# Kernel tuning notes

Hardware: AMD Instinct MI355X
Metric: run time of the kernel (lower is better)

The kernel has to match this reference:

```python
import jax, jax.numpy as jnp
import numpy as np

B, S, H = 2, 2048, 1024
E, K, I, IS = 8, 2, 1408, 2816

def setup_inputs() -> dict:
    key = jax.random.key(0)
    ks = jax.random.split(key, 9)
    sc = lambda fan_in: 1.0 / np.sqrt(fan_in)
    return {
        'hidden_states': jax.random.normal(ks[0], (B, S, H), jnp.float32),
        'gate_w': jax.random.normal(ks[1], (H, E), jnp.float32) * sc(H),
        'w_gate': jax.random.normal(ks[2], (E, H, I), jnp.float32) * sc(H),
        'w_up': jax.random.normal(ks[3], (E, H, I), jnp.float32) * sc(H),
        'w_down': jax.random.normal(ks[4], (E, I, H), jnp.float32) * sc(I),
        'sh_gate_w': jax.random.normal(ks[5], (H, IS), jnp.float32) * sc(H),
        'sh_up_w': jax.random.normal(ks[6], (H, IS), jnp.float32) * sc(H),
        'sh_down_w': jax.random.normal(ks[7], (IS, H), jnp.float32) * sc(IS),
        'sh_expert_gate_w': jax.random.normal(ks[8], (H, 1), jnp.float32) * sc(H),
        'top_k': K,
    }

def reference(hidden_states, gate_w, w_gate, w_up, w_down, sh_gate_w, sh_up_w, sh_down_w, sh_expert_gate_w, top_k):
    orig_shape = hidden_states.shape
    x = hidden_states.reshape(-1, orig_shape[-1])  # [T, H]
    T = x.shape[0]
    n_experts = gate_w.shape[1]
    # --- routing (matches _route_single_token, no expert_bias) ---
    logits = x @ gate_w                               # [T, E]
    topk_vals, topk_ids = jax.lax.top_k(logits, top_k)  # [T, K]
    topk_weights = jax.nn.softmax(topk_vals, axis=-1)   # [T, K]
    # dense routing matrix [T, E]; each token has K nonzeros
    route = jnp.zeros((T, n_experts), x.dtype).at[jnp.arange(T)[:, None], topk_ids].add(topk_weights)
    # --- expert SwiGLU FFNs, masked-combine over the fixed expert set ---
    out = jnp.zeros_like(x)
    for e in range(n_experts):
        h = jax.nn.silu(x @ w_gate[e]) * (x @ w_up[e])  # [T, I]
        out = out + route[:, e:e + 1] * (h @ w_down[e])
    # --- shared expert (always active) with sigmoid gate ---
    shared = (jax.nn.silu(x @ sh_gate_w) * (x @ sh_up_w)) @ sh_down_w
    shared = jax.nn.sigmoid(x @ sh_expert_gate_w) * shared
    out = out + shared
    return out.reshape(orig_shape)
```

## Files before the change

### kernel.cpp

```cpp
#include <hip/hip_runtime.h>
#include <hip/hip_bf16.h>

#define T_TOK 4096
#define HDIM  1024
#define NEXP  8
#define IDIM  1408
#define ISDIM 2816

typedef short bf16x8 __attribute__((ext_vector_type(8)));
typedef float f32x4  __attribute__((ext_vector_type(4)));
typedef unsigned short u16;
typedef unsigned short u16x4 __attribute__((ext_vector_type(4)));
typedef unsigned short u16x8 __attribute__((ext_vector_type(8)));

typedef __attribute__((address_space(1))) const void gvoid;
typedef __attribute__((address_space(3))) void lvoid;

__device__ __forceinline__ u16 f2bf(float f) {
    union { float f; unsigned u; } c; c.f = f;
    unsigned r = (c.u + 0x7FFFu + ((c.u >> 16) & 1u)) >> 16;
    return (u16)r;
}
__device__ __forceinline__ float bf2f(u16 v) {
    union { unsigned u; float f; } c; c.u = (unsigned)v << 16; return c.f;
}
__device__ __forceinline__ void glds16(const u16* g, u16* l) {
    __builtin_amdgcn_global_load_lds((gvoid*)g, (lvoid*)l, 16, 0, 0);
}

__global__ __launch_bounds__(256) void route_kernel(
    const float* __restrict__ X, const float* __restrict__ GW,
    const float* __restrict__ SEG,
    int* __restrict__ topk_e, float* __restrict__ topk_w,
    float* __restrict__ sgate)
{
    const int t = blockIdx.x * 4 + (threadIdx.x >> 6);
    const int lane = threadIdx.x & 63;
    float acc[NEXP];
    #pragma unroll
    for (int e = 0; e < NEXP; ++e) acc[e] = 0.f;
    float sacc = 0.f;
    const float* xr = X + (size_t)t * HDIM;
    for (int h = lane; h < HDIM; h += 64) {
        float xv = xr[h];
        f32x4 g0 = *(const f32x4*)(GW + (size_t)h * NEXP);
        f32x4 g1 = *(const f32x4*)(GW + (size_t)h * NEXP + 4);
        acc[0] += xv * g0[0]; acc[1] += xv * g0[1];
        acc[2] += xv * g0[2]; acc[3] += xv * g0[3];
        acc[4] += xv * g1[0]; acc[5] += xv * g1[1];
        acc[6] += xv * g1[2]; acc[7] += xv * g1[3];
        sacc += xv * SEG[h];
    }
    #pragma unroll
    for (int off = 32; off > 0; off >>= 1) {
        #pragma unroll
        for (int e = 0; e < NEXP; ++e) acc[e] += __shfl_down(acc[e], off);
        sacc += __shfl_down(sacc, off);
    }
    if (lane == 0) {
        int e0 = 0;
        #pragma unroll
        for (int e = 1; e < NEXP; ++e) if (acc[e] > acc[e0]) e0 = e;
        int e1 = (e0 == 0) ? 1 : 0;
        #pragma unroll
        for (int e = 0; e < NEXP; ++e)
            if (e != e0 && acc[e] > acc[e1]) e1 = e;
        float w0 = 1.f / (1.f + __expf(acc[e1] - acc[e0]));
        topk_e[t * 2]     = e0; topk_e[t * 2 + 1] = e1;
        topk_w[t * 2]     = w0; topk_w[t * 2 + 1] = 1.f - w0;
        sgate[t] = 1.f / (1.f + __expf(-sacc));
    }
}

__global__ __launch_bounds__(256) void hist_kernel(
    const int* __restrict__ topk_e, int* __restrict__ counts)
{
    __shared__ int h[NEXP];
    if (threadIdx.x < NEXP) h[threadIdx.x] = 0;
    __syncthreads();
    int i = blockIdx.x * 256 + threadIdx.x;
    atomicAdd(&h[topk_e[i]], 1);
    __syncthreads();
    if (threadIdx.x < NEXP) atomicAdd(&counts[threadIdx.x], h[threadIdx.x]);
}

__global__ void offsets_kernel(const int* __restrict__ counts,
                               int* __restrict__ seg_start,
                               int* __restrict__ cursors)
{
    if (threadIdx.x == 0) {
        int s = 0;
        for (int e = 0; e < NEXP; ++e) {
            seg_start[e] = s; cursors[e] = s; s += counts[e];
        }
    }
}

__global__ __launch_bounds__(256) void scatter_kernel(
    const int* __restrict__ topk_e,
    int* __restrict__ cursors, int* __restrict__ tok_ids,
    int* __restrict__ slot)
{
    const int i = blockIdx.x * 256 + threadIdx.x;
    const int lane = threadIdx.x & 63;
    const int e = topk_e[i];
    const unsigned long long lt = (1ull << lane) - 1ull;
    #pragma unroll
    for (int ex = 0; ex < NEXP; ++ex) {
        unsigned long long mask = __ballot(e == ex);
        if (mask == 0ull) continue;
        int cnt = __popcll(mask);
        int leader = __ffsll((long long)mask) - 1;
        int base_ = 0;
        if (lane == leader) base_ = atomicAdd(&cursors[ex], cnt);
        base_ = __shfl(base_, leader);
        if (e == ex) {
            int pos = base_ + __popcll(mask & lt);
            tok_ids[pos] = i >> 1;
            slot[i] = pos;
        }
    }
}

__global__ __launch_bounds__(256) void cvt_x_kernel(
    const float* __restrict__ in, u16* __restrict__ out, int n)
{
    int i = (blockIdx.x * 256 + threadIdx.x) * 8;
    if (i < n) {
        f32x4 a = *(const f32x4*)(in + i);
        f32x4 b = *(const f32x4*)(in + i + 4);
        u16x8 o;
        #pragma unroll
        for (int j = 0; j < 4; ++j) { o[j] = f2bf(a[j]); o[j + 4] = f2bf(b[j]); }
        *(u16x8*)(out + i) = o;
    }
}

__global__ __launch_bounds__(256) void transpose_cvt(
    const float* __restrict__ in0, const float* __restrict__ in1,
    u16* __restrict__ out, int K, int N, int split)
{
    const int z = blockIdx.z;
    const float* in = (z < split) ? (in0 + (size_t)z * K * N)
                                  : (in1 + (size_t)(z - split) * K * N);
    u16* o = out + (size_t)z * N * K;

    __shared__ float tile[64][65];
    const int n0 = blockIdx.x * 64, k0 = blockIdx.y * 64;
    const int tx = threadIdx.x & 15;
    const int ty = threadIdx.x >> 4;

    #pragma unroll
    for (int p = 0; p < 4; ++p) {
        int k = ty + p * 16;
        f32x4 v = *(const f32x4*)(in + (size_t)(k0 + k) * N + n0 + tx * 4);
        *(f32x4*)&tile[k][tx * 4] = v;
    }
    __syncthreads();
    #pragma unroll
    for (int p = 0; p < 4; ++p) {
        int n = ty + p * 16;
        u16x4 w;
        #pragma unroll
        for (int j = 0; j < 4; ++j) w[j] = f2bf(tile[tx * 4 + j][n]);
        *(u16x4*)(o + (size_t)(n0 + n) * K + k0 + tx * 4) = w;
    }
}

__global__ __launch_bounds__(256) void gemm_gu(
    const u16* __restrict__ A,
    const u16* __restrict__ Bg_, const u16* __restrict__ Bu_, size_t b_stride,
    u16* __restrict__ Hout,
    const int* __restrict__ a_ids, const int* __restrict__ seg_start,
    const int* __restrict__ counts,
    int N, int Trows)
{
    int e, m_tile, cnt, base;
    if (counts) {
        e = blockIdx.x; m_tile = blockIdx.y;
        cnt = counts[e]; base = seg_start[e];
    } else {
        e = 0; m_tile = blockIdx.x * gridDim.y + blockIdx.y;
        cnt = Trows; base = 0;
    }
    const int m0 = m_tile * 128;
    if (m0 >= cnt) return;
    const int n0 = blockIdx.z * 64;
    const u16* Bg = Bg_ + (size_t)e * b_stride;
    const u16* Bu = Bu_ + (size_t)e * b_stride;
    const int K = HDIM;

    __shared__ u16 As[2 * 4096];
    __shared__ u16 Bs[2 * 4096];

    const int tid = threadIdx.x;
    const int srow = tid >> 2;
    const int st_k = (tid & 3) * 8;
    int ar0 = m0 + srow;       if (ar0 >= cnt) ar0 = cnt - 1;
    int ar1 = m0 + srow + 64;  if (ar1 >= cnt) ar1 = cnt - 1;
    const int ga0 = a_ids ? a_ids[base + ar0] : (base + ar0);
    const int ga1 = a_ids ? a_ids[base + ar1] : (base + ar1);
    const u16* a0 = A + (size_t)ga0 * K + st_k;
    const u16* a1 = A + (size_t)ga1 * K + st_k;
    const u16* bg = Bg + (size_t)(n0 + srow) * K + st_k;
    const u16* bu = Bu + (size_t)(n0 + srow) * K + st_k;

    f32x4 accG[4][2], accU[4][2];
    #pragma unroll
    for (int i = 0; i < 4; ++i)
        #pragma unroll
        for (int j = 0; j < 2; ++j) {
            accG[i][j] = (f32x4){0.f, 0.f, 0.f, 0.f};
            accU[i][j] = (f32x4){0.f, 0.f, 0.f, 0.f};
        }

    const int lane = tid & 63;
    const int wv = tid >> 6;
    const int wr = (wv >> 1) * 64;
    const int wc = (wv & 1) * 32;
    const int lrow = lane & 15;
    const int lkb = (lane >> 4) * 8;

    int offA[4], offBg[2];
    #pragma unroll
    for (int m = 0; m < 4; ++m) offA[m] = (wr + m * 16 + lrow) * 32 + lkb;
    #pragma unroll
    for (int n = 0; n < 2; ++n) offBg[n] = (wc + n * 16 + lrow) * 32 + lkb;

#define STAGE_GU(ps) do { \
    glds16(a0, &As[(ps) + tid * 8]); \
    glds16(a1, &As[(ps) + 2048 + tid * 8]); \
    glds16(bg, &Bs[(ps) + tid * 8]); \
    glds16(bu, &Bs[(ps) + 2048 + tid * 8]); \
    a0 += 32; a1 += 32; bg += 32; bu += 32; } while (0)

#define COMPUTE_GU(ps) do { \
    bf16x8 af[4], bgf[2], bux[2]; \
    _Pragma("unroll") for (int m = 0; m < 4; ++m) af[m] = *(const bf16x8*)&As[(ps) + offA[m]]; \
    _Pragma("unroll") for (int n = 0; n < 2; ++n) { \
        bgf[n] = *(const bf16x8*)&Bs[(ps) + offBg[n]]; \
        bux[n] = *(const bf16x8*)&Bs[(ps) + offBg[n] + 2048]; } \
    _Pragma("unroll") for (int m = 0; m < 4; ++m) \
        _Pragma("unroll") for (int n = 0; n < 2; ++n) { \
            accG[m][n] = __builtin_amdgcn_mfma_f32_16x16x32_bf16(af[m], bgf[n], accG[m][n], 0, 0, 0); \
            accU[m][n] = __builtin_amdgcn_mfma_f32_16x16x32_bf16(af[m], bux[n], accU[m][n], 0, 0, 0); } \
    } while (0)

    STAGE_GU(0);
    STAGE_GU(4096);
    #pragma unroll 1
    for (int t = 0; t < 30; ++t) {
        asm volatile("s_waitcnt vmcnt(4)" ::: "memory");
        __builtin_amdgcn_s_barrier();
        const int ps = (t & 1) * 4096;
        COMPUTE_GU(ps);
        __builtin_amdgcn_s_barrier();
        STAGE_GU(ps);
    }
    asm volatile("s_waitcnt vmcnt(4)" ::: "memory");
    __builtin_amdgcn_s_barrier();
    COMPUTE_GU(0);
    asm volatile("s_waitcnt vmcnt(0)" ::: "memory");
    __builtin_amdgcn_s_barrier();
    COMPUTE_GU(4096);

    const int l4 = (lane >> 4) * 4;
    #pragma unroll
    for (int m = 0; m < 4; ++m)
        #pragma unroll
        for (int n = 0; n < 2; ++n)
            #pragma unroll
            for (int j = 0; j < 4; ++j) {
                int r = wr + m * 16 + l4 + j;
                if (m0 + r < cnt) {
                    int c = n0 + wc + n * 16 + lrow;
                    float g = accG[m][n][j], u = accU[m][n][j];
                    float hv = g / (1.f + __expf(-g)) * u;
                    Hout[(size_t)(base + m0 + r) * N + c] = f2bf(hv);
                }
            }
}

__global__ __launch_bounds__(256) void gemm_down(
    const u16* __restrict__ AE, const u16* __restrict__ AS,
    const u16* __restrict__ WDt, const u16* __restrict__ SDt,
    float* __restrict__ DexpO, float* __restrict__ OutS,
    const int* __restrict__ seg_start, const int* __restrict__ counts)
{
    const int zz = blockIdx.x;
    const bool shr = (zz >= 64);
    int n0, cnt, base, kstride;
    size_t koff;
    const u16 *Ab, *Be;
    if (!shr) {
        int e = zz & 7;
        n0 = (zz >> 3) * 128;
        cnt = counts[e]; base = seg_start[e];
        Ab = AE; Be = WDt + (size_t)e * (HDIM * IDIM);
        kstride = IDIM; koff = 0;
    } else {
        int idx = zz - 64;
        n0 = (idx & 7) * 128;
        cnt = T_TOK; base = 0;
        Ab = AS; Be = SDt;
        kstride = ISDIM; koff = (size_t)(idx >> 3) * 1408;
    }
    const int m0 = blockIdx.y * 128;
    if (m0 >= cnt) return;
    const int NT = 44;

    __shared__ u16 As[2 * 4096];
    __shared__ u16 Bs[2 * 4096];

    const int tid = threadIdx.x;
    const int srow = tid >> 2;
    const int st_k = (tid & 3) * 8;
    int ar0 = m0 + srow;       if (ar0 >= cnt) ar0 = cnt - 1;
    int ar1 = m0 + srow + 64;  if (ar1 >= cnt) ar1 = cnt - 1;
    const u16* a0 = Ab + (size_t)(base + ar0) * kstride + koff + st_k;
    const u16* a1 = Ab + (size_t)(base + ar1) * kstride + koff + st_k;
    const u16* b0 = Be + (size_t)(n0 + srow) * kstride + koff + st_k;
    const u16* b1 = Be + (size_t)(n0 + srow + 64) * kstride + koff + st_k;

    f32x4 acc[4][4];
    #pragma unroll
    for (int i = 0; i < 4; ++i)
        #pragma unroll
        for (int j = 0; j < 4; ++j) acc[i][j] = (f32x4){0.f, 0.f, 0.f, 0.f};

    const int lane = tid & 63;
    const int wv = tid >> 6;
    const int wr = (wv >> 1) * 64;
    const int wc = (wv & 1) * 64;
    const int lrow = lane & 15;
    const int lkb = (lane >> 4) * 8;

    int offA[4], offB[4];
    #pragma unroll
    for (int m = 0; m < 4; ++m) offA[m] = (wr + m * 16 + lrow) * 32 + lkb;
    #pragma unroll
    for (int n = 0; n < 4; ++n) offB[n] = (wc + n * 16 + lrow) * 32 + lkb;

#define STAGE_DN(ps) do { \
    glds16(a0, &As[(ps) + tid * 8]); \
    glds16(a1, &As[(ps) + 2048 + tid * 8]); \
    glds16(b0, &Bs[(ps) + tid * 8]); \
    glds16(b1, &Bs[(ps) + 2048 + tid * 8]); \
    a0 += 32; a1 += 32; b0 += 32; b1 += 32; } while (0)

#define COMPUTE_DN(ps) do { \
    bf16x8 af[4], bff[4]; \
    _Pragma("unroll") for (int m = 0; m < 4; ++m) af[m] = *(const bf16x8*)&As[(ps) + offA[m]]; \
    _Pragma("unroll") for (int n = 0; n < 4; ++n) bff[n] = *(const bf16x8*)&Bs[(ps) + offB[n]]; \
    _Pragma("unroll") for (int m = 0; m < 4; ++m) \
        _Pragma("unroll") for (int n = 0; n < 4; ++n) \
            acc[m][n] = __builtin_amdgcn_mfma_f32_16x16x32_bf16(af[m], bff[n], acc[m][n], 0, 0, 0); \
    } while (0)

    STAGE_DN(0);
    STAGE_DN(4096);
    #pragma unroll 1
    for (int t = 0; t < NT - 2; ++t) {
        asm volatile("s_waitcnt vmcnt(4)" ::: "memory");
        __builtin_amdgcn_s_barrier();
        const int ps = (t & 1) * 4096;
        COMPUTE_DN(ps);
        __builtin_amdgcn_s_barrier();
        STAGE_DN(ps);
    }
    asm volatile("s_waitcnt vmcnt(4)" ::: "memory");
    __builtin_amdgcn_s_barrier();
    COMPUTE_DN(0);
    asm volatile("s_waitcnt vmcnt(0)" ::: "memory");
    __builtin_amdgcn_s_barrier();
    COMPUTE_DN(4096);

    const int l4 = (lane >> 4) * 4;
    #pragma unroll
    for (int m = 0; m < 4; ++m)
        #pragma unroll
        for (int n = 0; n < 4; ++n)
            #pragma unroll
            for (int j = 0; j < 4; ++j) {
                int r = wr + m * 16 + l4 + j;
                if (m0 + r < cnt) {
                    int c = n0 + wc + n * 16 + lrow;
                    if (!shr)
                        DexpO[(size_t)(base + m0 + r) * HDIM + c] = acc[m][n][j];
                    else
                        atomicAdd(&OutS[(size_t)(m0 + r) * HDIM + c], acc[m][n][j]);
                }
            }
}

__global__ __launch_bounds__(256) void combine_kernel(
    const float* __restrict__ Dexp,
    const int* __restrict__ slot, const float* __restrict__ topk_w,
    const float* __restrict__ sgate, float* __restrict__ Out)
{
    int idx = blockIdx.x * 256 + threadIdx.x;
    int t = idx >> 8;
    int c = (idx & 255) * 4;
    int s0 = slot[2 * t], s1 = slot[2 * t + 1];
    float w0 = topk_w[2 * t], w1 = topk_w[2 * t + 1], sg = sgate[t];
    f32x4 sh = *(const f32x4*)(Out + (size_t)t * HDIM + c);
    f32x4 d0 = *(const f32x4*)(Dexp + (size_t)s0 * HDIM + c);
    f32x4 d1 = *(const f32x4*)(Dexp + (size_t)s1 * HDIM + c);
    f32x4 o;
    #pragma unroll
    for (int j = 0; j < 4; ++j) o[j] = sg * sh[j] + w0 * d0[j] + w1 * d1[j];
    *(f32x4*)(Out + (size_t)t * HDIM + c) = o;
}

extern "C" void kernel_launch(void* const* d_in, const int* in_sizes, int n_in,
                              void* d_out, int out_size, void* d_ws, size_t ws_size,
                              hipStream_t stream)
{
    const float* X   = (const float*)d_in[0];
    const float* GW  = (const float*)d_in[1];
    const float* WG  = (const float*)d_in[2];
    const float* WU  = (const float*)d_in[3];
    const float* WD  = (const float*)d_in[4];
    const float* SG  = (const float*)d_in[5];
    const float* SU  = (const float*)d_in[6];
    const float* SD  = (const float*)d_in[7];
    const float* SEG = (const float*)d_in[8];
    float* Out = (float*)d_out;

    char* ws = (char*)d_ws;
    int*   counts    = (int*)(ws + 0);
    int*   seg_start = (int*)(ws + 64);
    int*   cursors   = (int*)(ws + 128);
    int*   topk_e    = (int*)(ws + 1024);
    float* topk_w    = (float*)(ws + 1024 + 32768);
    float* sgate     = (float*)(ws + 1024 + 65536);
    int*   tok_ids   = (int*)(ws + 1024 + 65536 + 16384);
    int*   slot      = (int*)(ws + 1024 + 65536 + 16384 + 32768);

    u16* Xbf  = (u16*)(ws + 0x40000ull);
    u16* Hact = (u16*)(ws + 0xA00000ull);
    u16* Hs   = (u16*)(ws + 0x2200000ull);
    u16* WGUt = (u16*)(ws + 0x3A00000ull);
    u16* WDt  = (u16*)(ws + 0x6900000ull);
    u16* SGUt = (u16*)(ws + 0x8100000ull);
    u16* SDt  = (u16*)(ws + 0x8D00000ull);
    u16* WGt = WGUt;
    u16* WUt = WGUt + (size_t)NEXP * IDIM * HDIM;
    u16* SGt = SGUt;
    u16* SUt = SGUt + (size_t)ISDIM * HDIM;
    float* Dexp = (float*)(ws + 0x3A00000ull);

    hipMemsetAsync(counts, 0, 64, stream);
    hipMemsetAsync(Out, 0, (size_t)T_TOK * HDIM * sizeof(float), stream);

    route_kernel<<<T_TOK / 4, 256, 0, stream>>>(X, GW, SEG, topk_e, topk_w, sgate);
    hist_kernel<<<(T_TOK * 2) / 256, 256, 0, stream>>>(topk_e, counts);
    offsets_kernel<<<1, 64, 0, stream>>>(counts, seg_start, cursors);
    scatter_kernel<<<(T_TOK * 2) / 256, 256, 0, stream>>>(topk_e, cursors, tok_ids, slot);

    cvt_x_kernel<<<(T_TOK * HDIM) / (256 * 8), 256, 0, stream>>>(X, Xbf, T_TOK * HDIM);
    transpose_cvt<<<dim3(IDIM / 64, HDIM / 64, 2 * NEXP), 256, 0, stream>>>(WG, WU, WGUt, HDIM, IDIM, NEXP);
    transpose_cvt<<<dim3(HDIM / 64, IDIM / 64, NEXP), 256, 0, stream>>>(WD, WD, WDt, IDIM, HDIM, NEXP);
    transpose_cvt<<<dim3(ISDIM / 64, HDIM / 64, 2), 256, 0, stream>>>(SG, SU, SGUt, HDIM, ISDIM, 1);
    transpose_cvt<<<dim3(HDIM / 64, ISDIM / 64, 1), 256, 0, stream>>>(SD, SD, SDt, ISDIM, HDIM, 1);

    gemm_gu<<<dim3(NEXP, T_TOK / 128, IDIM / 64), 256, 0, stream>>>(
        Xbf, WGt, WUt, (size_t)IDIM * HDIM, Hact,
        tok_ids, seg_start, counts, IDIM, 0);
    gemm_gu<<<dim3(8, T_TOK / 128 / 8, ISDIM / 64), 256, 0, stream>>>(
        Xbf, SGt, SUt, 0, Hs,
        nullptr, nullptr, nullptr, ISDIM, T_TOK);

    gemm_down<<<dim3(80, T_TOK / 128), 256, 0, stream>>>(
        Hact, Hs, WDt, SDt, Dexp, Out,
        seg_start, counts);

    combine_kernel<<<(T_TOK * HDIM / 4) / 256, 256, 0, stream>>>(
        Dexp, slot, topk_w, sgate, Out);
}
```

Before: 342.4 us.

## Enlarge GEMM tiles to 256x256 with interleaved gate/up weights and swizzled LDS

The gate/up and down GEMMs move from 128-row tiles with 256 threads to 256x256 tiles with 512 threads, BK=64 and a 128KB dynamic LDS double buffer. Gate and up weight rows are interleaved in 16-row groups during the transpose, so a single B tile carries both, and the epilogue pairs adjacent fragments for SwiGLU. LDS reads use an XOR swizzle to avoid bank conflicts, and MFMA bursts run at raised wave priority. The aim is more reuse per loaded byte and fewer tiles, at the cost of more padding waste on small expert segments, higher register pressure and lower occupancy.

```diff
diff --git a/kernel.cpp b/kernel.cpp
--- a/kernel.cpp
+++ b/kernel.cpp
@@ -138,12 +138,15 @@
 
 __global__ __launch_bounds__(256) void transpose_cvt(
     const float* __restrict__ in0, const float* __restrict__ in1,
-    u16* __restrict__ out, int K, int N, int split)
+    u16* __restrict__ out, int K, int N, int split, int ilv)
 {
     const int z = blockIdx.z;
+    const int e = (z < split) ? z : z - split;
     const float* in = (z < split) ? (in0 + (size_t)z * K * N)
                                   : (in1 + (size_t)(z - split) * K * N);
-    u16* o = out + (size_t)z * N * K;
+    u16* o = ilv ? (out + (size_t)e * 2 * N * K)
+                 : (out + (size_t)z * N * K);
+    const int radd = ilv ? ((z < split) ? 0 : 16) : 0;
 
     __shared__ float tile[64][65];
     const int n0 = blockIdx.x * 64, k0 = blockIdx.y * 64;
@@ -163,232 +166,228 @@
         u16x4 w;
         #pragma unroll
         for (int j = 0; j < 4; ++j) w[j] = f2bf(tile[tx * 4 + j][n]);
-        *(u16x4*)(o + (size_t)(n0 + n) * K + k0 + tx * 4) = w;
-    }
-}
-
-__global__ __launch_bounds__(256) void gemm_gu(
-    const u16* __restrict__ A,
-    const u16* __restrict__ Bg_, const u16* __restrict__ Bu_, size_t b_stride,
+        int R = n0 + n;
+        int orow = ilv ? (((R >> 4) * 32) + (R & 15) + radd) : R;
+        *(u16x4*)(o + (size_t)orow * K + k0 + tx * 4) = w;
+    }
+}
+
+
+#define MFMA16(MB, AV, BV) \
+    _Pragma("unroll") for (int m_ = 0; m_ < 4; ++m_) \
+        _Pragma("unroll") for (int n_ = 0; n_ < 4; ++n_) \
+            acc[(MB) + m_][n_] = __builtin_amdgcn_mfma_f32_16x16x32_bf16(AV[m_], BV[n_], acc[(MB) + m_][n_], 0, 0, 0);
+
+#define COMP256(bufo) do { \
+    bf16x8 av[4], bv[4]; \
+    _Pragma("unroll") for (int m_ = 0; m_ < 4; ++m_) av[m_] = *(const bf16x8*)&As[(bufo) + aof + m_ * 1024]; \
+    _Pragma("unroll") for (int n_ = 0; n_ < 4; ++n_) bv[n_] = *(const bf16x8*)&Bs[(bufo) + bof + n_ * 1024]; \
+    __builtin_amdgcn_s_setprio(1); MFMA16(0, av, bv) __builtin_amdgcn_s_setprio(0); \
+    _Pragma("unroll") for (int m_ = 0; m_ < 4; ++m_) av[m_] = *(const bf16x8*)&As[(bufo) + aof + (m_ + 4) * 1024]; \
+    __builtin_amdgcn_s_setprio(1); MFMA16(4, av, bv) __builtin_amdgcn_s_setprio(0); \
+    _Pragma("unroll") for (int m_ = 0; m_ < 4; ++m_) av[m_] = *(const bf16x8*)&As[(bufo) + (aof ^ 32) + m_ * 1024]; \
+    _Pragma("unroll") for (int n_ = 0; n_ < 4; ++n_) bv[n_] = *(const bf16x8*)&Bs[(bufo) + (bof ^ 32) + n_ * 1024]; \
+    __builtin_amdgcn_s_setprio(1); MFMA16(0, av, bv) __builtin_amdgcn_s_setprio(0); \
+    _Pragma("unroll") for (int m_ = 0; m_ < 4; ++m_) av[m_] = *(const bf16x8*)&As[(bufo) + (aof ^ 32) + (m_ + 4) * 1024]; \
+    __builtin_amdgcn_s_setprio(1); MFMA16(4, av, bv) __builtin_amdgcn_s_setprio(0); \
+} while (0)
+
+#define STAGE256() do { \
+    glds16(ap0, &As[stbuf + tid * 8]); \
+    glds16(ap1, &As[stbuf + 4096 + tid * 8]); \
+    glds16(ap2, &As[stbuf + 8192 + tid * 8]); \
+    glds16(ap3, &As[stbuf + 12288 + tid * 8]); \
+    glds16(bp0, &Bs[stbuf + tid * 8]); \
+    glds16(bp1, &Bs[stbuf + 4096 + tid * 8]); \
+    glds16(bp2, &Bs[stbuf + 8192 + tid * 8]); \
+    glds16(bp3, &Bs[stbuf + 12288 + tid * 8]); \
+    ap0 += 64; ap1 += 64; ap2 += 64; ap3 += 64; \
+    bp0 += 64; bp1 += 64; bp2 += 64; bp3 += 64; \
+    stbuf ^= 16384; } while (0)
+
+#define GEMM_LOOP(NT) \
+    STAGE256(); STAGE256(); \
+    _Pragma("unroll 1") \
+    for (int t = 0; t < (NT) - 2; ++t) { \
+        asm volatile("s_waitcnt vmcnt(8)" ::: "memory"); \
+        __builtin_amdgcn_s_barrier(); \
+        COMP256((t & 1) * 16384); \
+        __builtin_amdgcn_s_barrier(); \
+        STAGE256(); \
+    } \
+    asm volatile("s_waitcnt vmcnt(8)" ::: "memory"); \
+    __builtin_amdgcn_s_barrier(); \
+    COMP256(0); \
+    asm volatile("s_waitcnt vmcnt(0)" ::: "memory"); \
+    __builtin_amdgcn_s_barrier(); \
+    COMP256(16384);
+
+__global__ __launch_bounds__(512, 2) void gemm_gu(
+    const u16* __restrict__ A, const u16* __restrict__ Bc_, size_t b_stride,
     u16* __restrict__ Hout,
     const int* __restrict__ a_ids, const int* __restrict__ seg_start,
-    const int* __restrict__ counts,
-    int N, int Trows)
-{
-    int e, m_tile, cnt, base;
+    const int* __restrict__ counts, int Nout)
+{
+    extern __shared__ u16 lds[];
+    u16* As = lds;
+    u16* Bs = lds + 32768;
+
+    int e, m0, cnt, base;
     if (counts) {
-        e = blockIdx.x; m_tile = blockIdx.y;
+        e = blockIdx.x; m0 = blockIdx.y * 256;
         cnt = counts[e]; base = seg_start[e];
     } else {
-        e = 0; m_tile = blockIdx.x * gridDim.y + blockIdx.y;
-        cnt = Trows; base = 0;
-    }
-    const int m0 = m_tile * 128;
+        e = 0; m0 = (blockIdx.x * gridDim.y + blockIdx.y) * 256;
+        cnt = T_TOK; base = 0;
+    }
     if (m0 >= cnt) return;
-    const int n0 = blockIdx.z * 64;
-    const u16* Bg = Bg_ + (size_t)e * b_stride;
-    const u16* Bu = Bu_ + (size_t)e * b_stride;
+    const u16* Bsrc = Bc_ + (size_t)e * b_stride;
     const int K = HDIM;
-
-    __shared__ u16 As[2 * 4096];
-    __shared__ u16 Bs[2 * 4096];
+    const int n0e = blockIdx.z * 256;
 
     const int tid = threadIdx.x;
-    const int srow = tid >> 2;
-    const int st_k = (tid & 3) * 8;
-    int ar0 = m0 + srow;       if (ar0 >= cnt) ar0 = cnt - 1;
-    int ar1 = m0 + srow + 64;  if (ar1 >= cnt) ar1 = cnt - 1;
-    const int ga0 = a_ids ? a_ids[base + ar0] : (base + ar0);
-    const int ga1 = a_ids ? a_ids[base + ar1] : (base + ar1);
-    const u16* a0 = A + (size_t)ga0 * K + st_k;
-    const u16* a1 = A + (size_t)ga1 * K + st_k;
-    const u16* bg = Bg + (size_t)(n0 + srow) * K + st_k;
-    const u16* bu = Bu + (size_t)(n0 + srow) * K + st_k;
-
-    f32x4 accG[4][2], accU[4][2];
-    #pragma unroll
-    for (int i = 0; i < 4; ++i)
-        #pragma unroll
-        for (int j = 0; j < 2; ++j) {
-            accG[i][j] = (f32x4){0.f, 0.f, 0.f, 0.f};
-            accU[i][j] = (f32x4){0.f, 0.f, 0.f, 0.f};
-        }
+    const int srow = tid >> 3;
+    const int sw = ((tid & 7) ^ (srow & 7)) * 8;
+
+    const u16 *ap0, *ap1, *ap2, *ap3, *bp0, *bp1, *bp2, *bp3;
+    {
+        int r0 = m0 + srow;       if (r0 >= cnt) r0 = cnt - 1;
+        int r1 = m0 + 64 + srow;  if (r1 >= cnt) r1 = cnt - 1;
+        int r2 = m0 + 128 + srow; if (r2 >= cnt) r2 = cnt - 1;
+        int r3 = m0 + 192 + srow; if (r3 >= cnt) r3 = cnt - 1;
+        int g0 = a_ids ? a_ids[base + r0] : (base + r0);
+        int g1 = a_ids ? a_ids[base + r1] : (base + r1);
+        int g2 = a_ids ? a_ids[base + r2] : (base + r2);
+        int g3 = a_ids ? a_ids[base + r3] : (base + r3);
+        ap0 = A + (size_t)g0 * K + sw;
+        ap1 = A + (size_t)g1 * K + sw;
+        ap2 = A + (size_t)g2 * K + sw;
+        ap3 = A + (size_t)g3 * K + sw;
+        bp0 = Bsrc + (size_t)(n0e + srow) * K + sw;
+        bp1 = Bsrc + (size_t)(n0e + 64 + srow) * K + sw;
+        bp2 = Bsrc + (size_t)(n0e + 128 + srow) * K + sw;
+        bp3 = Bsrc + (size_t)(n0e + 192 + srow) * K + sw;
+    }
+    int stbuf = 0;
+
+    f32x4 acc[8][4];
+    #pragma unroll
+    for (int i = 0; i < 8; ++i)
+        #pragma unroll
+        for (int j = 0; j < 4; ++j) acc[i][j] = (f32x4){0.f, 0.f, 0.f, 0.f};
 
     const int lane = tid & 63;
     const int wv = tid >> 6;
-    const int wr = (wv >> 1) * 64;
-    const int wc = (wv & 1) * 32;
+    const int wr = wv >> 2;
+    const int wn = wv & 3;
     const int lrow = lane & 15;
-    const int lkb = (lane >> 4) * 8;
-
-    int offA[4], offBg[2];
-    #pragma unroll
-    for (int m = 0; m < 4; ++m) offA[m] = (wr + m * 16 + lrow) * 32 + lkb;
-    #pragma unroll
-    for (int n = 0; n < 2; ++n) offBg[n] = (wc + n * 16 + lrow) * 32 + lkb;
-
-#define STAGE_GU(ps) do { \
-    glds16(a0, &As[(ps) + tid * 8]); \
-    glds16(a1, &As[(ps) + 2048 + tid * 8]); \
-    glds16(bg, &Bs[(ps) + tid * 8]); \
-    glds16(bu, &Bs[(ps) + 2048 + tid * 8]); \
-    a0 += 32; a1 += 32; bg += 32; bu += 32; } while (0)
-
-#define COMPUTE_GU(ps) do { \
-    bf16x8 af[4], bgf[2], bux[2]; \
-    _Pragma("unroll") for (int m = 0; m < 4; ++m) af[m] = *(const bf16x8*)&As[(ps) + offA[m]]; \
-    _Pragma("unroll") for (int n = 0; n < 2; ++n) { \
-        bgf[n] = *(const bf16x8*)&Bs[(ps) + offBg[n]]; \
-        bux[n] = *(const bf16x8*)&Bs[(ps) + offBg[n] + 2048]; } \
-    _Pragma("unroll") for (int m = 0; m < 4; ++m) \
-        _Pragma("unroll") for (int n = 0; n < 2; ++n) { \
-            accG[m][n] = __builtin_amdgcn_mfma_f32_16x16x32_bf16(af[m], bgf[n], accG[m][n], 0, 0, 0); \
-            accU[m][n] = __builtin_amdgcn_mfma_f32_16x16x32_bf16(af[m], bux[n], accU[m][n], 0, 0, 0); } \
-    } while (0)
-
-    STAGE_GU(0);
-    STAGE_GU(4096);
-    #pragma unroll 1
-    for (int t = 0; t < 30; ++t) {
-        asm volatile("s_waitcnt vmcnt(4)" ::: "memory");
-        __builtin_amdgcn_s_barrier();
-        const int ps = (t & 1) * 4096;
-        COMPUTE_GU(ps);
-        __builtin_amdgcn_s_barrier();
-        STAGE_GU(ps);
-    }
-    asm volatile("s_waitcnt vmcnt(4)" ::: "memory");
-    __builtin_amdgcn_s_barrier();
-    COMPUTE_GU(0);
-    asm volatile("s_waitcnt vmcnt(0)" ::: "memory");
-    __builtin_amdgcn_s_barrier();
-    COMPUTE_GU(4096);
-
-    const int l4 = (lane >> 4) * 4;
-    #pragma unroll
-    for (int m = 0; m < 4; ++m)
-        #pragma unroll
-        for (int n = 0; n < 2; ++n)
+    const int kslot = lane >> 4;
+    const int aof = (wr * 128 + lrow) * 64 + ((kslot ^ (lrow & 7)) * 8);
+    const int bof = (wn * 64 + lrow) * 64 + ((kslot ^ (lrow & 7)) * 8);
+
+    GEMM_LOOP(16)
+
+    const int l4 = kslot * 4;
+    #pragma unroll
+    for (int mf = 0; mf < 8; ++mf)
+        #pragma unroll
+        for (int p = 0; p < 2; ++p) {
+            f32x4 g = acc[mf][2 * p], u = acc[mf][2 * p + 1];
+            int ci = blockIdx.z * 128 + (wn * 2 + p) * 16 + lrow;
             #pragma unroll
             for (int j = 0; j < 4; ++j) {
-                int r = wr + m * 16 + l4 + j;
-                if (m0 + r < cnt) {
-                    int c = n0 + wc + n * 16 + lrow;
-                    float g = accG[m][n][j], u = accU[m][n][j];
-                    float hv = g / (1.f + __expf(-g)) * u;
-                    Hout[(size_t)(base + m0 + r) * N + c] = f2bf(hv);
+                int r = m0 + wr * 128 + mf * 16 + l4 + j;
+                if (r < cnt) {
+                    float hv = g[j] / (1.f + __expf(-g[j])) * u[j];
+                    Hout[(size_t)(base + r) * Nout + ci] = f2bf(hv);
                 }
             }
-}
-
-__global__ __launch_bounds__(256) void gemm_down(
+        }
+}
+
+__global__ __launch_bounds__(512, 2) void gemm_down(
     const u16* __restrict__ AE, const u16* __restrict__ AS,
     const u16* __restrict__ WDt, const u16* __restrict__ SDt,
     float* __restrict__ DexpO, float* __restrict__ OutS,
     const int* __restrict__ seg_start, const int* __restrict__ counts)
 {
+    extern __shared__ u16 lds[];
+    u16* As = lds;
+    u16* Bs = lds + 32768;
+
     const int zz = blockIdx.x;
-    const bool shr = (zz >= 64);
-    int n0, cnt, base, kstride;
+    const bool shr = (zz >= 32);
+    int n0, cnt, base, kst;
     size_t koff;
-    const u16 *Ab, *Be;
+    const u16 *Asrc, *Bsrc;
     if (!shr) {
         int e = zz & 7;
-        n0 = (zz >> 3) * 128;
+        n0 = (zz >> 3) * 256;
         cnt = counts[e]; base = seg_start[e];
-        Ab = AE; Be = WDt + (size_t)e * (HDIM * IDIM);
-        kstride = IDIM; koff = 0;
+        Asrc = AE; Bsrc = WDt + (size_t)e * (HDIM * IDIM);
+        kst = IDIM; koff = 0;
     } else {
-        int idx = zz - 64;
-        n0 = (idx & 7) * 128;
+        int idx = zz - 32;
+        n0 = (idx & 3) * 256;
         cnt = T_TOK; base = 0;
-        Ab = AS; Be = SDt;
-        kstride = ISDIM; koff = (size_t)(idx >> 3) * 1408;
-    }
-    const int m0 = blockIdx.y * 128;
+        Asrc = AS; Bsrc = SDt;
+        kst = ISDIM; koff = (size_t)(idx >> 2) * 1408;
+    }
+    const int m0 = blockIdx.y * 256;
     if (m0 >= cnt) return;
-    const int NT = 44;
-
-    __shared__ u16 As[2 * 4096];
-    __shared__ u16 Bs[2 * 4096];
 
     const int tid = threadIdx.x;
-    const int srow = tid >> 2;
-    const int st_k = (tid & 3) * 8;
-    int ar0 = m0 + srow;       if (ar0 >= cnt) ar0 = cnt - 1;
-    int ar1 = m0 + srow + 64;  if (ar1 >= cnt) ar1 = cnt - 1;
-    const u16* a0 = Ab + (size_t)(base + ar0) * kstride + koff + st_k;
-    const u16* a1 = Ab + (size_t)(base + ar1) * kstride + koff + st_k;
-    const u16* b0 = Be + (size_t)(n0 + srow) * kstride + koff + st_k;
-    const u16* b1 = Be + (size_t)(n0 + srow + 64) * kstride + koff + st_k;
-
-    f32x4 acc[4][4];
-    #pragma unroll
-    for (int i = 0; i < 4; ++i)
+    const int srow = tid >> 3;
+    const int sw = ((tid & 7) ^ (srow & 7)) * 8;
+
+    const u16 *ap0, *ap1, *ap2, *ap3, *bp0, *bp1, *bp2, *bp3;
+    {
+        int r0 = m0 + srow;       if (r0 >= cnt) r0 = cnt - 1;
+        int r1 = m0 + 64 + srow;  if (r1 >= cnt) r1 = cnt - 1;
+        int r2 = m0 + 128 + srow; if (r2 >= cnt) r2 = cnt - 1;
+        int r3 = m0 + 192 + srow; if (r3 >= cnt) r3 = cnt - 1;
+        ap0 = Asrc + (size_t)(base + r0) * kst + koff + sw;
+        ap1 = Asrc + (size_t)(base + r1) * kst + koff + sw;
+        ap2 = Asrc + (size_t)(base + r2) * kst + koff + sw;
+        ap3 = Asrc + (size_t)(base + r3) * kst + koff + sw;
+        bp0 = Bsrc + (size_t)(n0 + srow) * kst + koff + sw;
+        bp1 = Bsrc + (size_t)(n0 + 64 + srow) * kst + koff + sw;
+        bp2 = Bsrc + (size_t)(n0 + 128 + srow) * kst + koff + sw;
+        bp3 = Bsrc + (size_t)(n0 + 192 + srow) * kst + koff + sw;
+    }
+    int stbuf = 0;
+
+    f32x4 acc[8][4];
+    #pragma unroll
+    for (int i = 0; i < 8; ++i)
         #pragma unroll
         for (int j = 0; j < 4; ++j) acc[i][j] = (f32x4){0.f, 0.f, 0.f, 0.f};
 
     const int lane = tid & 63;
     const int wv = tid >> 6;
-    const int wr = (wv >> 1) * 64;
-    const int wc = (wv & 1) * 64;
+    const int wr = wv >> 2;
+    const int wn = wv & 3;
     const int lrow = lane & 15;
-    const int lkb = (lane >> 4) * 8;
-
-    int offA[4], offB[4];
-    #pragma unroll
-    for (int m = 0; m < 4; ++m) offA[m] = (wr + m * 16 + lrow) * 32 + lkb;
-    #pragma unroll
-    for (int n = 0; n < 4; ++n) offB[n] = (wc + n * 16 + lrow) * 32 + lkb;
-
-#define STAGE_DN(ps) do { \
-    glds16(a0, &As[(ps) + tid * 8]); \
-    glds16(a1, &As[(ps) + 2048 + tid * 8]); \
-    glds16(b0, &Bs[(ps) + tid * 8]); \
-    glds16(b1, &Bs[(ps) + 2048 + tid * 8]); \
-    a0 += 32; a1 += 32; b0 += 32; b1 += 32; } while (0)
-
-#define COMPUTE_DN(ps) do { \
-    bf16x8 af[4], bff[4]; \
-    _Pragma("unroll") for (int m = 0; m < 4; ++m) af[m] = *(const bf16x8*)&As[(ps) + offA[m]]; \
-    _Pragma("unroll") for (int n = 0; n < 4; ++n) bff[n] = *(const bf16x8*)&Bs[(ps) + offB[n]]; \
-    _Pragma("unroll") for (int m = 0; m < 4; ++m) \
-        _Pragma("unroll") for (int n = 0; n < 4; ++n) \
-            acc[m][n] = __builtin_amdgcn_mfma_f32_16x16x32_bf16(af[m], bff[n], acc[m][n], 0, 0, 0); \
-    } while (0)
-
-    STAGE_DN(0);
-    STAGE_DN(4096);
-    #pragma unroll 1
-    for (int t = 0; t < NT - 2; ++t) {
-        asm volatile("s_waitcnt vmcnt(4)" ::: "memory");
-        __builtin_amdgcn_s_barrier();
-        const int ps = (t & 1) * 4096;
-        COMPUTE_DN(ps);
-        __builtin_amdgcn_s_barrier();
-        STAGE_DN(ps);
-    }
-    asm volatile("s_waitcnt vmcnt(4)" ::: "memory");
-    __builtin_amdgcn_s_barrier();
-    COMPUTE_DN(0);
-    asm volatile("s_waitcnt vmcnt(0)" ::: "memory");
-    __builtin_amdgcn_s_barrier();
-    COMPUTE_DN(4096);
-
-    const int l4 = (lane >> 4) * 4;
-    #pragma unroll
-    for (int m = 0; m < 4; ++m)
-        #pragma unroll
-        for (int n = 0; n < 4; ++n)
+    const int kslot = lane >> 4;
+    const int aof = (wr * 128 + lrow) * 64 + ((kslot ^ (lrow & 7)) * 8);
+    const int bof = (wn * 64 + lrow) * 64 + ((kslot ^ (lrow & 7)) * 8);
+
+    GEMM_LOOP(22)
+
+    const int l4 = kslot * 4;
+    #pragma unroll
+    for (int mf = 0; mf < 8; ++mf)
+        #pragma unroll
+        for (int nf = 0; nf < 4; ++nf)
             #pragma unroll
             for (int j = 0; j < 4; ++j) {
-                int r = wr + m * 16 + l4 + j;
-                if (m0 + r < cnt) {
-                    int c = n0 + wc + n * 16 + lrow;
+                int r = m0 + wr * 128 + mf * 16 + l4 + j;
+                if (r < cnt) {
+                    int c = n0 + wn * 64 + nf * 16 + lrow;
                     if (!shr)
-                        DexpO[(size_t)(base + m0 + r) * HDIM + c] = acc[m][n][j];
+                        DexpO[(size_t)(base + r) * HDIM + c] = acc[mf][nf][j];
                     else
-                        atomicAdd(&OutS[(size_t)(m0 + r) * HDIM + c], acc[m][n][j]);
+                        atomicAdd(&OutS[(size_t)r * HDIM + c], acc[mf][nf][j]);
                 }
             }
 }
@@ -440,14 +439,10 @@
     u16* Xbf  = (u16*)(ws + 0x40000ull);
     u16* Hact = (u16*)(ws + 0xA00000ull);
     u16* Hs   = (u16*)(ws + 0x2200000ull);
-    u16* WGUt = (u16*)(ws + 0x3A00000ull);
+    u16* WGUc = (u16*)(ws + 0x3A00000ull);
     u16* WDt  = (u16*)(ws + 0x6900000ull);
-    u16* SGUt = (u16*)(ws + 0x8100000ull);
+    u16* SGUc = (u16*)(ws + 0x8100000ull);
     u16* SDt  = (u16*)(ws + 0x8D00000ull);
-    u16* WGt = WGUt;
-    u16* WUt = WGUt + (size_t)NEXP * IDIM * HDIM;
-    u16* SGt = SGUt;
-    u16* SUt = SGUt + (size_t)ISDIM * HDIM;
     float* Dexp = (float*)(ws + 0x3A00000ull);
 
     hipMemsetAsync(counts, 0, 64, stream);
@@ -459,19 +454,19 @@
     scatter_kernel<<<(T_TOK * 2) / 256, 256, 0, stream>>>(topk_e, cursors, tok_ids, slot);
 
     cvt_x_kernel<<<(T_TOK * HDIM) / (256 * 8), 256, 0, stream>>>(X, Xbf, T_TOK * HDIM);
-    transpose_cvt<<<dim3(IDIM / 64, HDIM / 64, 2 * NEXP), 256, 0, stream>>>(WG, WU, WGUt, HDIM, IDIM, NEXP);
-    transpose_cvt<<<dim3(HDIM / 64, IDIM / 64, NEXP), 256, 0, stream>>>(WD, WD, WDt, IDIM, HDIM, NEXP);
-    transpose_cvt<<<dim3(ISDIM / 64, HDIM / 64, 2), 256, 0, stream>>>(SG, SU, SGUt, HDIM, ISDIM, 1);
-    transpose_cvt<<<dim3(HDIM / 64, ISDIM / 64, 1), 256, 0, stream>>>(SD, SD, SDt, ISDIM, HDIM, 1);
-
-    gemm_gu<<<dim3(NEXP, T_TOK / 128, IDIM / 64), 256, 0, stream>>>(
-        Xbf, WGt, WUt, (size_t)IDIM * HDIM, Hact,
-        tok_ids, seg_start, counts, IDIM, 0);
-    gemm_gu<<<dim3(8, T_TOK / 128 / 8, ISDIM / 64), 256, 0, stream>>>(
-        Xbf, SGt, SUt, 0, Hs,
-        nullptr, nullptr, nullptr, ISDIM, T_TOK);
-
-    gemm_down<<<dim3(80, T_TOK / 128), 256, 0, stream>>>(
+    transpose_cvt<<<dim3(IDIM / 64, HDIM / 64, 2 * NEXP), 256, 0, stream>>>(WG, WU, WGUc, HDIM, IDIM, NEXP, 1);
+    transpose_cvt<<<dim3(HDIM / 64, IDIM / 64, NEXP), 256, 0, stream>>>(WD, WD, WDt, IDIM, HDIM, NEXP, 0);
+    transpose_cvt<<<dim3(ISDIM / 64, HDIM / 64, 2), 256, 0, stream>>>(SG, SU, SGUc, HDIM, ISDIM, 1, 1);
+    transpose_cvt<<<dim3(HDIM / 64, ISDIM / 64, 1), 256, 0, stream>>>(SD, SD, SDt, ISDIM, HDIM, 1, 0);
+
+    gemm_gu<<<dim3(NEXP, 16, 11), 512, 131072, stream>>>(
+        Xbf, WGUc, (size_t)2 * IDIM * HDIM, Hact,
+        tok_ids, seg_start, counts, IDIM);
+    gemm_gu<<<dim3(8, 2, 22), 512, 131072, stream>>>(
+        Xbf, SGUc, 0, Hs,
+        nullptr, nullptr, nullptr, ISDIM);
+
+    gemm_down<<<dim3(40, 16), 512, 131072, stream>>>(
         Hact, Hs, WDt, SDt, Dexp, Out,
         seg_start, counts);
 
```

Result: slower. 363.2 us (+6.1%).

## Triple-buffer LDS staging and XOR-swizzle k-chunks in both MoE GEMMs

Applied to the files above, without the earlier changes.

Both the gate/up GEMM and the down GEMM move from double to triple LDS buffering, which keeps two k-tiles of global-to-LDS loads in flight (vmcnt 8) while the current tile is computed. The loop tail is extended so the last three tiles drain correctly. The 8-element k-chunk positions are XOR-swizzled by row on the global load side and matched on the fragment read side, so MFMA operand reads from LDS should hit fewer bank conflicts. The cost is 1.5x the shared memory per block (48KB), which may lower occupancy, plus modulo-3 buffer indexing.

```diff
diff --git a/kernel.cpp b/kernel.cpp
--- a/kernel.cpp
+++ b/kernel.cpp
@@ -167,6 +167,7 @@
     }
 }
 
+
 __global__ __launch_bounds__(256) void gemm_gu(
     const u16* __restrict__ A,
     const u16* __restrict__ Bg_, const u16* __restrict__ Bu_, size_t b_stride,
@@ -190,12 +191,12 @@
     const u16* Bu = Bu_ + (size_t)e * b_stride;
     const int K = HDIM;
 
-    __shared__ u16 As[2 * 4096];
-    __shared__ u16 Bs[2 * 4096];
+    __shared__ u16 As[3 * 4096];
+    __shared__ u16 Bs[3 * 4096];
 
     const int tid = threadIdx.x;
     const int srow = tid >> 2;
-    const int st_k = (tid & 3) * 8;
+    const int st_k = ((tid & 3) ^ (srow & 3)) * 8;
     int ar0 = m0 + srow;       if (ar0 >= cnt) ar0 = cnt - 1;
     int ar1 = m0 + srow + 64;  if (ar1 >= cnt) ar1 = cnt - 1;
     const int ga0 = a_ids ? a_ids[base + ar0] : (base + ar0);
@@ -219,13 +220,14 @@
     const int wr = (wv >> 1) * 64;
     const int wc = (wv & 1) * 32;
     const int lrow = lane & 15;
-    const int lkb = (lane >> 4) * 8;
+    const int kslot = lane >> 4;
+    const int ksw = (kslot ^ (lrow & 3)) * 8;
 
     int offA[4], offBg[2];
     #pragma unroll
-    for (int m = 0; m < 4; ++m) offA[m] = (wr + m * 16 + lrow) * 32 + lkb;
-    #pragma unroll
-    for (int n = 0; n < 2; ++n) offBg[n] = (wc + n * 16 + lrow) * 32 + lkb;
+    for (int m = 0; m < 4; ++m) offA[m] = (wr + m * 16 + lrow) * 32 + ksw;
+    #pragma unroll
+    for (int n = 0; n < 2; ++n) offBg[n] = (wc + n * 16 + lrow) * 32 + ksw;
 
 #define STAGE_GU(ps) do { \
     glds16(a0, &As[(ps) + tid * 8]); \
@@ -246,17 +248,19 @@
             accU[m][n] = __builtin_amdgcn_mfma_f32_16x16x32_bf16(af[m], bux[n], accU[m][n], 0, 0, 0); } \
     } while (0)
 
-    STAGE_GU(0);
-    STAGE_GU(4096);
+    STAGE_GU(0); STAGE_GU(4096); STAGE_GU(8192);
     #pragma unroll 1
-    for (int t = 0; t < 30; ++t) {
-        asm volatile("s_waitcnt vmcnt(4)" ::: "memory");
+    for (int t = 0; t < 32 - 3; ++t) {
+        asm volatile("s_waitcnt vmcnt(8)" ::: "memory");
         __builtin_amdgcn_s_barrier();
-        const int ps = (t & 1) * 4096;
+        const int ps = (t % 3) * 4096;
         COMPUTE_GU(ps);
         __builtin_amdgcn_s_barrier();
         STAGE_GU(ps);
     }
+    asm volatile("s_waitcnt vmcnt(8)" ::: "memory");
+    __builtin_amdgcn_s_barrier();
+    COMPUTE_GU(8192);
     asm volatile("s_waitcnt vmcnt(4)" ::: "memory");
     __builtin_amdgcn_s_barrier();
     COMPUTE_GU(0);
@@ -264,7 +268,7 @@
     __builtin_amdgcn_s_barrier();
     COMPUTE_GU(4096);
 
-    const int l4 = (lane >> 4) * 4;
+    const int l4 = kslot * 4;
     #pragma unroll
     for (int m = 0; m < 4; ++m)
         #pragma unroll
@@ -307,14 +311,13 @@
     }
     const int m0 = blockIdx.y * 128;
     if (m0 >= cnt) return;
-    const int NT = 44;
-
-    __shared__ u16 As[2 * 4096];
-    __shared__ u16 Bs[2 * 4096];
+
+    __shared__ u16 As[3 * 4096];
+    __shared__ u16 Bs[3 * 4096];
 
     const int tid = threadIdx.x;
     const int srow = tid >> 2;
-    const int st_k = (tid & 3) * 8;
+    const int st_k = ((tid & 3) ^ (srow & 3)) * 8;
     int ar0 = m0 + srow;       if (ar0 >= cnt) ar0 = cnt - 1;
     int ar1 = m0 + srow + 64;  if (ar1 >= cnt) ar1 = cnt - 1;
     const u16* a0 = Ab + (size_t)(base + ar0) * kstride + koff + st_k;
@@ -333,13 +336,14 @@
     const int wr = (wv >> 1) * 64;
     const int wc = (wv & 1) * 64;
     const int lrow = lane & 15;
-    const int lkb = (lane >> 4) * 8;
+    const int kslot = lane >> 4;
+    const int ksw = (kslot ^ (lrow & 3)) * 8;
 
     int offA[4], offB[4];
     #pragma unroll
-    for (int m = 0; m < 4; ++m) offA[m] = (wr + m * 16 + lrow) * 32 + lkb;
-    #pragma unroll
-    for (int n = 0; n < 4; ++n) offB[n] = (wc + n * 16 + lrow) * 32 + lkb;
+    for (int m = 0; m < 4; ++m) offA[m] = (wr + m * 16 + lrow) * 32 + ksw;
+    #pragma unroll
+    for (int n = 0; n < 4; ++n) offB[n] = (wc + n * 16 + lrow) * 32 + ksw;
 
 #define STAGE_DN(ps) do { \
     glds16(a0, &As[(ps) + tid * 8]); \
@@ -357,17 +361,19 @@
             acc[m][n] = __builtin_amdgcn_mfma_f32_16x16x32_bf16(af[m], bff[n], acc[m][n], 0, 0, 0); \
     } while (0)
 
-    STAGE_DN(0);
-    STAGE_DN(4096);
+    STAGE_DN(0); STAGE_DN(4096); STAGE_DN(8192);
     #pragma unroll 1
-    for (int t = 0; t < NT - 2; ++t) {
-        asm volatile("s_waitcnt vmcnt(4)" ::: "memory");
+    for (int t = 0; t < 44 - 3; ++t) {
+        asm volatile("s_waitcnt vmcnt(8)" ::: "memory");
         __builtin_amdgcn_s_barrier();
-        const int ps = (t & 1) * 4096;
+        const int ps = (t % 3) * 4096;
         COMPUTE_DN(ps);
         __builtin_amdgcn_s_barrier();
         STAGE_DN(ps);
     }
+    asm volatile("s_waitcnt vmcnt(8)" ::: "memory");
+    __builtin_amdgcn_s_barrier();
+    COMPUTE_DN(8192);
     asm volatile("s_waitcnt vmcnt(4)" ::: "memory");
     __builtin_amdgcn_s_barrier();
     COMPUTE_DN(0);
@@ -375,7 +381,7 @@
     __builtin_amdgcn_s_barrier();
     COMPUTE_DN(4096);
 
-    const int l4 = (lane >> 4) * 4;
+    const int l4 = kslot * 4;
     #pragma unroll
     for (int m = 0; m < 4; ++m)
         #pragma unroll
```

Result: no change. 348.3 us (+1.7%).
